# Performance work log

Measured on AMD Instinct MI355X. Metric: run time of the kernel, lower is better.

Reference implementation:

```python
import jax, jax.numpy as jnp
import numpy as np

B, C, H, W = 32, 256, 32, 32
C8 = C // 8


def setup_inputs() -> dict:
    key = jax.random.key(0)
    ks = jax.random.split(key, 8)
    s = 1.0 / np.sqrt(C)
    return {
        "x": jax.random.normal(ks[0], (B, C, H, W), dtype=jnp.float32),
        "Wq": jax.random.normal(ks[1], (C8, C), dtype=jnp.float32) * s,
        "bq": jax.random.normal(ks[2], (C8,), dtype=jnp.float32) * s,
        "Wk": jax.random.normal(ks[3], (C8, C), dtype=jnp.float32) * s,
        "bk": jax.random.normal(ks[4], (C8,), dtype=jnp.float32) * s,
        "Wv": jax.random.normal(ks[5], (C, C), dtype=jnp.float32) * s,
        "bv": jax.random.normal(ks[6], (C,), dtype=jnp.float32) * s,
        "gamma": jax.random.normal(ks[7], (1,), dtype=jnp.float32) * 0.1,
    }


def reference(x, Wq, bq, Wk, bk, Wv, bv, gamma):
    b, c, h, w = x.shape
    n = h * w
    xf = x.reshape(b, c, n)  # [B, C, N]
    # 1x1 convs == per-pixel linear projections
    q = jnp.einsum('dc,bcn->bnd', Wq, xf) + bq            # [B, N, C/8]
    k = jnp.einsum('dc,bcn->bdn', Wk, xf) + bk[:, None]    # [B, C/8, N]
    v = jnp.einsum('dc,bcn->bdn', Wv, xf) + bv[:, None]    # [B, C, N]
    energy = jnp.einsum('bnd,bdm->bnm', q, k)              # [B, N, N], no scaling (as in source)
    attn = jax.nn.softmax(energy, axis=-1)                 # softmax over keys
    # out[:, :, i] = sum_j V[:, :, j] * attn[i, j]
    out = jnp.einsum('bdn,bmn->bdm', v, attn)              # [B, C, N]
    out = out.reshape(b, c, h, w)
    return gamma * out + x
```

## Files before the change

### kernel.cpp

```cpp
#include <hip/hip_runtime.h>
#include <math.h>

#define BB 32
#define CC 256
#define CQ 32
#define NN 1024

typedef short bf16x8 __attribute__((ext_vector_type(8)));
typedef float f32x4  __attribute__((ext_vector_type(4)));
typedef unsigned short u16;

__device__ __forceinline__ u16 f2bf(float f) {
    unsigned u = __float_as_uint(f);
    u = (u + 0x7FFFu + ((u >> 16) & 1u)) >> 16;
    return (u16)u;
}

__device__ __forceinline__ unsigned cvt_pk_bf16(float lo, float hi) {
    unsigned r;
    asm("v_cvt_pk_bf16_f32 %0, %1, %2" : "=v"(r) : "v"(lo), "v"(hi));
    return r;
}

__global__ void wpack_kernel(const float* __restrict__ Wq,
                             const float* __restrict__ Wk,
                             const float* __restrict__ Wv,
                             u16* __restrict__ wfrag)
{
    const int o = blockIdx.x * 256 + threadIdx.x;
    const int j    = o & 7;
    const int lane = (o >> 3) & 63;
    const int kc   = (o >> 9) & 7;
    const int rt   = o >> 12;
    const int row  = rt * 16 + (lane & 15);
    const int col  = kc * 32 + (lane >> 4) * 8 + j;
    const float v = (row < 32) ? Wq[row * 256 + col]
                  : (row < 64) ? Wk[(row - 32) * 256 + col]
                               : Wv[(row - 64) * 256 + col];
    wfrag[o] = f2bf(v);
}

struct QSmem {
    union {
        u16 xs[32][268];
        u16 osv[CC][40];
    };
    u16 osqk[32][72];
};

__global__ __launch_bounds__(256, 4) void qkv_kernel(
    const float* __restrict__ x, const u16* __restrict__ wfrag,
    const float* __restrict__ bq, const float* __restrict__ bk,
    const float* __restrict__ bv,
    u16* __restrict__ qt, u16* __restrict__ kt, u16* __restrict__ vv)
{
    __shared__ QSmem sm;
    const int b = blockIdx.y, n0 = blockIdx.x * 32;
    const int t = threadIdx.x;
    const int lane = t & 63, w = t >> 6;
    const int quad = lane >> 4, c16 = lane & 15;

    {
        const float* xb = x + (size_t)b * CC * NN + n0;
        const int n4 = (t & 7) * 4;
        const int cr = t >> 3;
        float4 f[8];
#pragma unroll
        for (int it = 0; it < 8; ++it)
            f[it] = *(const float4*)(xb + (size_t)(it * 32 + cr) * NN + n4);
#pragma unroll
        for (int it = 0; it < 8; ++it) {
            const int c = it * 32 + cr;
            sm.xs[n4 + 0][c] = f2bf(f[it].x);
            sm.xs[n4 + 1][c] = f2bf(f[it].y);
            sm.xs[n4 + 2][c] = f2bf(f[it].z);
            sm.xs[n4 + 3][c] = f2bf(f[it].w);
        }
    }
    __syncthreads();

    f32x4 acc[5][2];
#pragma unroll
    for (int i = 0; i < 5; ++i)
#pragma unroll
        for (int j = 0; j < 2; ++j) acc[i][j] = (f32x4){0.f, 0.f, 0.f, 0.f};

#pragma unroll 2
    for (int k = 0; k < 8; ++k) {
        const int c0 = k * 32;
        bf16x8 wa[5], xb[2];
#pragma unroll
        for (int rs = 0; rs < 5; ++rs)
            wa[rs] = *(const bf16x8*)&wfrag[(size_t)(((w * 5 + rs) * 8 + k) * 64 + lane) * 8];
#pragma unroll
        for (int ns = 0; ns < 2; ++ns) {
            const short4 a = *(const short4*)&sm.xs[ns * 16 + c16][c0 + quad * 8];
            const short4 b2 = *(const short4*)&sm.xs[ns * 16 + c16][c0 + quad * 8 + 4];
            bf16x8 v;
            v[0] = a.x; v[1] = a.y; v[2] = a.z; v[3] = a.w;
            v[4] = b2.x; v[5] = b2.y; v[6] = b2.z; v[7] = b2.w;
            xb[ns] = v;
        }
#pragma unroll
        for (int rs = 0; rs < 5; ++rs)
#pragma unroll
            for (int ns = 0; ns < 2; ++ns)
                acc[rs][ns] = __builtin_amdgcn_mfma_f32_16x16x32_bf16(
                    wa[rs], xb[ns], acc[rs][ns], 0, 0, 0);
    }

    __syncthreads();

#pragma unroll
    for (int rs = 0; rs < 5; ++rs) {
#pragma unroll
        for (int r = 0; r < 4; ++r) {
            const int rg = w * 80 + rs * 16 + quad * 4 + r;
            const float bias = (rg < 32) ? bq[rg] : (rg < 64) ? bk[rg - 32] : bv[rg - 64];
#pragma unroll
            for (int ns = 0; ns < 2; ++ns) {
                const int n = ns * 16 + c16;
                const u16 h = f2bf(acc[rs][ns][r] + bias);
                if (rg < 64) sm.osqk[n][rg] = h;
                else         sm.osv[rg - 64][n] = h;
            }
        }
    }
    __syncthreads();

    {
        u16* dst = (t >= 128) ? kt : qt;
        const int dof = (t >= 128) ? 32 : 0;
        const int o = (t & 127) * 8;
        const int n = o >> 5, d = o & 31;
        const bf16x8 v = *(const bf16x8*)&sm.osqk[n][d + dof];
        *(bf16x8*)&dst[((size_t)b * NN + n0) * CQ + o] = v;
    }
#pragma unroll
    for (int it = 0; it < 4; ++it) {
        const int o = it * 2048 + t * 8;
        const int c = o >> 5, n = o & 31;
        const bf16x8 v = *(const bf16x8*)&sm.osv[c][n];
        *(bf16x8*)&vv[((size_t)b * CC + c) * NN + n0 + n] = v;
    }
}

__global__ __launch_bounds__(512, 4) void attn_kernel(
    const u16* __restrict__ qt, const u16* __restrict__ kt,
    const u16* __restrict__ vv, const float* __restrict__ x,
    const float* __restrict__ gamma_p, float* __restrict__ out)
{
    __shared__ u16 ps16[2][64][136];
    __shared__ float lsh[64];

    const int bid  = blockIdx.x;
    const int xcd  = bid & 7;
    const int slot = bid >> 3;
    const int b    = (xcd << 2) | (slot >> 4);
    const int m0   = (slot & 15) * 64;

    const int t = threadIdx.x, lane = t & 63, w = t >> 6;
    const int quad = lane >> 4, c16 = lane & 15;
    const int ch   = c16 >> 3;
    const int c7   = c16 & 7;
    const int qkey = (c16 >> 2) & 3;
    const int sm   = w & 3;
    const int sh   = w >> 2;
    const int ms0  = w & 3;

    const bf16x8 qa = *(const bf16x8*)&qt[((size_t)b * NN + m0 + sm * 16 + c16) * CQ + quad * 8];

    bf16x8 ones;
#pragma unroll
    for (int j = 0; j < 8; ++j) ones[j] = (short)0x3F80;

    f32x4 accO[2][4];
    f32x4 lsum = (f32x4){0.f, 0.f, 0.f, 0.f};
#pragma unroll
    for (int cs = 0; cs < 2; ++cs)
#pragma unroll
        for (int j = 0; j < 4; ++j) accO[cs][j] = (f32x4){0.f, 0.f, 0.f, 0.f};

    const u16* vbase = vv + (size_t)b * CC * NN;
    const u16* kbase = kt + (size_t)b * NN * CQ;

    bf16x8 kb[4];
#pragma unroll
    for (int s = 0; s < 4; ++s)
        kb[s] = *(const bf16x8*)&kbase[(size_t)(sh * 64 + s * 16 + c16) * CQ + quad * 8];

    for (int step = 0; step < 8; ++step) {
        const int nbase = step * 128;
        u16* psb = &ps16[step & 1][0][0];

        bf16x8 va[2][4];
#pragma unroll
        for (int cs = 0; cs < 2; ++cs)
#pragma unroll
            for (int kc = 0; kc < 4; ++kc)
                va[cs][kc] = *(const bf16x8*)&vbase[
                    (size_t)(w * 32 + cs * 16 + c16) * NN + nbase + kc * 32 + quad * 8];

        f32x4 accS[4];
#pragma unroll
        for (int s = 0; s < 4; ++s)
            accS[s] = __builtin_amdgcn_mfma_f32_16x16x32_bf16(
                qa, kb[s], (f32x4){0.f, 0.f, 0.f, 0.f}, 0, 0, 0);

        const int rowb = sm * 16 + quad * 4;
#pragma unroll
        for (int s = 0; s < 4; ++s) {
            const int nbt = sh * 8 + 2 * s + ch;
            const int p = nbt ^ quad;
            u16* pw = &psb[rowb * 136 + p * 8 + c7];
            const float e0 = __expf(accS[s][0]);
            const float e1 = __expf(accS[s][1]);
            const float e2 = __expf(accS[s][2]);
            const float e3 = __expf(accS[s][3]);
            const unsigned p01 = cvt_pk_bf16(e0, e1);
            const unsigned p23 = cvt_pk_bf16(e2, e3);
            pw[0]   = (u16)p01;
            pw[136] = (u16)(p01 >> 16);
            pw[272] = (u16)p23;
            pw[408] = (u16)(p23 >> 16);
        }

        if (step < 7) {
#pragma unroll
            for (int s = 0; s < 4; ++s)
                kb[s] = *(const bf16x8*)&kbase[
                    (size_t)(nbase + 128 + sh * 64 + s * 16 + c16) * CQ + quad * 8];
        }

        asm volatile("s_waitcnt lgkmcnt(0)" ::: "memory");
        __builtin_amdgcn_s_barrier();
        asm volatile("" ::: "memory");

        __builtin_amdgcn_s_setprio(1);
#pragma unroll
        for (int msi = 0; msi < 4; ++msi) {
            bf16x8 pb[4];
#pragma unroll
            for (int kc = 0; kc < 4; ++kc)
                pb[kc] = *(const bf16x8*)&psb[(msi * 16 + c16) * 136
                                              + (4 * kc + (quad ^ qkey)) * 8];
            if (msi == ms0) {
#pragma unroll
                for (int kc = 0; kc < 4; ++kc)
                    lsum = __builtin_amdgcn_mfma_f32_16x16x32_bf16(ones, pb[kc], lsum, 0, 0, 0);
            }
#pragma unroll
            for (int cs = 0; cs < 2; ++cs)
#pragma unroll
                for (int kc = 0; kc < 4; ++kc)
                    accO[cs][msi] = __builtin_amdgcn_mfma_f32_16x16x32_bf16(
                        va[cs][kc], pb[kc], accO[cs][msi], 0, 0, 0);
        }
        __builtin_amdgcn_s_setprio(0);
    }

    if (sh == 0 && quad == 0) lsh[ms0 * 16 + c16] = lsum[0];
    __syncthreads();

    const float gamma = gamma_p[0];
#pragma unroll
    for (int ms = 0; ms < 4; ++ms) {
        const float inv = gamma / lsh[ms * 16 + c16];
        const int m = m0 + ms * 16 + c16;
#pragma unroll
        for (int cs = 0; cs < 2; ++cs) {
            const int cbase = w * 32 + cs * 16 + quad * 4;
#pragma unroll
            for (int r = 0; r < 4; ++r) {
                const size_t idx = ((size_t)b * CC + cbase + r) * NN + m;
                out[idx] = accO[cs][ms][r] * inv + x[idx];
            }
        }
    }
}

extern "C" void kernel_launch(void* const* d_in, const int* in_sizes, int n_in,
                              void* d_out, int out_size, void* d_ws, size_t ws_size,
                              hipStream_t stream)
{
    const float* x  = (const float*)d_in[0];
    const float* Wq = (const float*)d_in[1];
    const float* bq = (const float*)d_in[2];
    const float* Wk = (const float*)d_in[3];
    const float* bk = (const float*)d_in[4];
    const float* Wv = (const float*)d_in[5];
    const float* bv = (const float*)d_in[6];
    const float* gm = (const float*)d_in[7];
    float* out = (float*)d_out;

    u16* qt    = (u16*)d_ws;
    u16* kt    = qt + (size_t)BB * NN * CQ;
    u16* vv    = kt + (size_t)BB * NN * CQ;
    u16* wfrag = vv + (size_t)BB * CC * NN;

    wpack_kernel<<<320, 256, 0, stream>>>(Wq, Wk, Wv, wfrag);
    dim3 grid(32, BB);
    qkv_kernel<<<grid, 256, 0, stream>>>(x, wfrag, bq, bk, bv, qt, kt, vv);
    attn_kernel<<<512, 512, 0, stream>>>(qt, kt, vv, x, gm, out);
}
```

Baseline: 150.9 us.

## Fuse weight packing into QKV kernel and halve attention key tile

Removes the separate weight-packing kernel launch. The QKV kernel now loads fp32 weights directly and converts them to bf16 inside its k-loop, which it no longer unrolls. The attention kernel drops from 128-key steps to 64-key steps, halving shared-memory P buffers and register use. It also replaces the manual lgkmcnt wait, barrier and setprio with __syncthreads. This trades one launch and less LDS/registers for more redundant fp32 weight reads and conversions per block and twice as many barriers in attention.

```diff
diff --git a/kernel.cpp b/kernel.cpp
--- a/kernel.cpp
+++ b/kernel.cpp
@@ -20,24 +20,6 @@
     unsigned r;
     asm("v_cvt_pk_bf16_f32 %0, %1, %2" : "=v"(r) : "v"(lo), "v"(hi));
     return r;
-}
-
-__global__ void wpack_kernel(const float* __restrict__ Wq,
-                             const float* __restrict__ Wk,
-                             const float* __restrict__ Wv,
-                             u16* __restrict__ wfrag)
-{
-    const int o = blockIdx.x * 256 + threadIdx.x;
-    const int j    = o & 7;
-    const int lane = (o >> 3) & 63;
-    const int kc   = (o >> 9) & 7;
-    const int rt   = o >> 12;
-    const int row  = rt * 16 + (lane & 15);
-    const int col  = kc * 32 + (lane >> 4) * 8 + j;
-    const float v = (row < 32) ? Wq[row * 256 + col]
-                  : (row < 64) ? Wk[(row - 32) * 256 + col]
-                               : Wv[(row - 64) * 256 + col];
-    wfrag[o] = f2bf(v);
 }
 
 struct QSmem {
@@ -49,7 +31,9 @@
 };
 
 __global__ __launch_bounds__(256, 4) void qkv_kernel(
-    const float* __restrict__ x, const u16* __restrict__ wfrag,
+    const float* __restrict__ x,
+    const float* __restrict__ Wq, const float* __restrict__ Wk,
+    const float* __restrict__ Wv,
     const float* __restrict__ bq, const float* __restrict__ bk,
     const float* __restrict__ bv,
     u16* __restrict__ qt, u16* __restrict__ kt, u16* __restrict__ vv)
@@ -79,19 +63,36 @@
     }
     __syncthreads();
 
+    const float* wsrc[5];
+#pragma unroll
+    for (int rs = 0; rs < 5; ++rs) {
+        const int rt = w * 5 + rs;
+        wsrc[rs] = (rt < 2) ? &Wq[(rt * 16 + c16) * 256]
+                 : (rt < 4) ? &Wk[((rt - 2) * 16 + c16) * 256]
+                            : &Wv[((rt - 4) * 16 + c16) * 256];
+    }
+
     f32x4 acc[5][2];
 #pragma unroll
     for (int i = 0; i < 5; ++i)
 #pragma unroll
         for (int j = 0; j < 2; ++j) acc[i][j] = (f32x4){0.f, 0.f, 0.f, 0.f};
 
-#pragma unroll 2
+#pragma unroll 1
     for (int k = 0; k < 8; ++k) {
         const int c0 = k * 32;
         bf16x8 wa[5], xb[2];
 #pragma unroll
-        for (int rs = 0; rs < 5; ++rs)
-            wa[rs] = *(const bf16x8*)&wfrag[(size_t)(((w * 5 + rs) * 8 + k) * 64 + lane) * 8];
+        for (int rs = 0; rs < 5; ++rs) {
+            const float4 f0 = *(const float4*)&wsrc[rs][c0 + quad * 8];
+            const float4 f1 = *(const float4*)&wsrc[rs][c0 + quad * 8 + 4];
+            union { unsigned u[4]; bf16x8 v; } wu;
+            wu.u[0] = cvt_pk_bf16(f0.x, f0.y);
+            wu.u[1] = cvt_pk_bf16(f0.z, f0.w);
+            wu.u[2] = cvt_pk_bf16(f1.x, f1.y);
+            wu.u[3] = cvt_pk_bf16(f1.z, f1.w);
+            wa[rs] = wu.v;
+        }
 #pragma unroll
         for (int ns = 0; ns < 2; ++ns) {
             const short4 a = *(const short4*)&sm.xs[ns * 16 + c16][c0 + quad * 8];
@@ -150,7 +151,7 @@
     const u16* __restrict__ vv, const float* __restrict__ x,
     const float* __restrict__ gamma_p, float* __restrict__ out)
 {
-    __shared__ u16 ps16[2][64][136];
+    __shared__ u16 ps16[2][64][68];
     __shared__ float lsh[64];
 
     const int bid  = blockIdx.x;
@@ -184,35 +185,34 @@
     const u16* vbase = vv + (size_t)b * CC * NN;
     const u16* kbase = kt + (size_t)b * NN * CQ;
 
-    bf16x8 kb[4];
-#pragma unroll
-    for (int s = 0; s < 4; ++s)
-        kb[s] = *(const bf16x8*)&kbase[(size_t)(sh * 64 + s * 16 + c16) * CQ + quad * 8];
-
-    for (int step = 0; step < 8; ++step) {
-        const int nbase = step * 128;
+    bf16x8 kb[2];
+#pragma unroll
+    for (int s = 0; s < 2; ++s)
+        kb[s] = *(const bf16x8*)&kbase[(size_t)(sh * 32 + s * 16 + c16) * CQ + quad * 8];
+
+    for (int step = 0; step < 16; ++step) {
+        const int nbase = step * 64;
         u16* psb = &ps16[step & 1][0][0];
 
-        bf16x8 va[2][4];
+        bf16x8 va[2][2];
 #pragma unroll
         for (int cs = 0; cs < 2; ++cs)
 #pragma unroll
-            for (int kc = 0; kc < 4; ++kc)
+            for (int kc = 0; kc < 2; ++kc)
                 va[cs][kc] = *(const bf16x8*)&vbase[
                     (size_t)(w * 32 + cs * 16 + c16) * NN + nbase + kc * 32 + quad * 8];
 
-        f32x4 accS[4];
-#pragma unroll
-        for (int s = 0; s < 4; ++s)
+        f32x4 accS[2];
+#pragma unroll
+        for (int s = 0; s < 2; ++s)
             accS[s] = __builtin_amdgcn_mfma_f32_16x16x32_bf16(
                 qa, kb[s], (f32x4){0.f, 0.f, 0.f, 0.f}, 0, 0, 0);
 
         const int rowb = sm * 16 + quad * 4;
 #pragma unroll
-        for (int s = 0; s < 4; ++s) {
-            const int nbt = sh * 8 + 2 * s + ch;
-            const int p = nbt ^ quad;
-            u16* pw = &psb[rowb * 136 + p * 8 + c7];
+        for (int s = 0; s < 2; ++s) {
+            const int nb = (sh * 4 + 2 * s + ch) ^ quad;
+            u16* pw = &psb[rowb * 68 + nb * 8 + c7];
             const float e0 = __expf(accS[s][0]);
             const float e1 = __expf(accS[s][1]);
             const float e2 = __expf(accS[s][2]);
@@ -220,43 +220,38 @@
             const unsigned p01 = cvt_pk_bf16(e0, e1);
             const unsigned p23 = cvt_pk_bf16(e2, e3);
             pw[0]   = (u16)p01;
-            pw[136] = (u16)(p01 >> 16);
-            pw[272] = (u16)p23;
-            pw[408] = (u16)(p23 >> 16);
-        }
-
-        if (step < 7) {
-#pragma unroll
-            for (int s = 0; s < 4; ++s)
+            pw[68]  = (u16)(p01 >> 16);
+            pw[136] = (u16)p23;
+            pw[204] = (u16)(p23 >> 16);
+        }
+
+        if (step < 15) {
+#pragma unroll
+            for (int s = 0; s < 2; ++s)
                 kb[s] = *(const bf16x8*)&kbase[
-                    (size_t)(nbase + 128 + sh * 64 + s * 16 + c16) * CQ + quad * 8];
-        }
-
-        asm volatile("s_waitcnt lgkmcnt(0)" ::: "memory");
-        __builtin_amdgcn_s_barrier();
-        asm volatile("" ::: "memory");
-
-        __builtin_amdgcn_s_setprio(1);
+                    (size_t)(nbase + 64 + sh * 32 + s * 16 + c16) * CQ + quad * 8];
+        }
+
+        __syncthreads();
+
 #pragma unroll
         for (int msi = 0; msi < 4; ++msi) {
-            bf16x8 pb[4];
-#pragma unroll
-            for (int kc = 0; kc < 4; ++kc)
-                pb[kc] = *(const bf16x8*)&psb[(msi * 16 + c16) * 136
+            bf16x8 pb[2];
+#pragma unroll
+            for (int kc = 0; kc < 2; ++kc)
+                pb[kc] = *(const bf16x8*)&psb[(msi * 16 + c16) * 68
                                               + (4 * kc + (quad ^ qkey)) * 8];
             if (msi == ms0) {
-#pragma unroll
-                for (int kc = 0; kc < 4; ++kc)
-                    lsum = __builtin_amdgcn_mfma_f32_16x16x32_bf16(ones, pb[kc], lsum, 0, 0, 0);
+                lsum = __builtin_amdgcn_mfma_f32_16x16x32_bf16(ones, pb[0], lsum, 0, 0, 0);
+                lsum = __builtin_amdgcn_mfma_f32_16x16x32_bf16(ones, pb[1], lsum, 0, 0, 0);
             }
 #pragma unroll
             for (int cs = 0; cs < 2; ++cs)
 #pragma unroll
-                for (int kc = 0; kc < 4; ++kc)
+                for (int kc = 0; kc < 2; ++kc)
                     accO[cs][msi] = __builtin_amdgcn_mfma_f32_16x16x32_bf16(
                         va[cs][kc], pb[kc], accO[cs][msi], 0, 0, 0);
         }
-        __builtin_amdgcn_s_setprio(0);
     }
 
     if (sh == 0 && quad == 0) lsh[ms0 * 16 + c16] = lsum[0];
@@ -293,13 +288,11 @@
     const float* gm = (const float*)d_in[7];
     float* out = (float*)d_out;
 
-    u16* qt    = (u16*)d_ws;
-    u16* kt    = qt + (size_t)BB * NN * CQ;
-    u16* vv    = kt + (size_t)BB * NN * CQ;
-    u16* wfrag = vv + (size_t)BB * CC * NN;
-
-    wpack_kernel<<<320, 256, 0, stream>>>(Wq, Wk, Wv, wfrag);
+    u16* qt = (u16*)d_ws;
+    u16* kt = qt + (size_t)BB * NN * CQ;
+    u16* vv = kt + (size_t)BB * NN * CQ;
+
     dim3 grid(32, BB);
-    qkv_kernel<<<grid, 256, 0, stream>>>(x, wfrag, bq, bk, bv, qt, kt, vv);
+    qkv_kernel<<<grid, 256, 0, stream>>>(x, Wq, Wk, Wv, bq, bk, bv, qt, kt, vv);
     attn_kernel<<<512, 512, 0, stream>>>(qt, kt, vv, x, gm, out);
 }
```

Measured after the change: 199.8 us. +32.4%, slower.
